# Kernel optimization log

Measured on AMD Instinct MI355X. Metric: run time of the kernel, lower is better.

The kernel has to match this reference:

```python
import jax, jax.numpy as jnp
import numpy as np

B, T, D = 8, 2048, 768
NUM_HEADS, KEY_DIM, VAL_DIM = 12, 64, 64
QKV_OUT = NUM_HEADS * (2 * KEY_DIM + VAL_DIM)  # 2304
MHK = NUM_HEADS * KEY_DIM  # 768


def setup_inputs() -> dict:
    key = jax.random.key(0)
    k = jax.random.split(key, 5)
    x = jax.random.normal(k[0], (B, T, D), dtype=jnp.float32)
    # Linear weights stored as [in, out] (equivalent to torch W.T)
    w_qkv = jax.random.normal(k[1], (D, QKV_OUT), dtype=jnp.float32) * (1.0 / np.sqrt(D))
    b_qkv = jax.random.normal(k[2], (QKV_OUT,), dtype=jnp.float32) * 0.02
    w_out = jax.random.normal(k[3], (NUM_HEADS * VAL_DIM, D), dtype=jnp.float32) * (1.0 / np.sqrt(NUM_HEADS * VAL_DIM))
    b_out = jax.random.normal(k[4], (D,), dtype=jnp.float32) * 0.02
    return {"x": x, "w_qkv": w_qkv, "b_qkv": b_qkv, "w_out": w_out, "b_out": b_out}


def reference(x, w_qkv, b_qkv, w_out, b_out):
    # qkv: [B, T, 2304]
    qkv = jnp.einsum('btd,de->bte', x, w_qkv) + b_qkv
    q = qkv[:, :, :MHK]            # [B, T, 768]
    k = qkv[:, :, MHK:2 * MHK]     # [B, T, 768]
    v = qkv[:, :, 2 * MHK:]        # [B, T, 768]
    # NOTE: faithful to source — contracts over the FULL num_heads*key_dim dim
    # (no head split), scale = sqrt(key_dim) only.
    scores = jnp.einsum('bqd,bkd->bqk', q, k) / jnp.sqrt(jnp.float32(KEY_DIM))
    attn = jax.nn.softmax(scores, axis=-1)        # [B, T, T]
    out = jnp.einsum('bqk,bkd->bqd', attn, v)      # [B, T, 768]
    return jnp.einsum('btd,de->bte', out, w_out) + b_out
```

## Files before the change

kernel.cpp:

```cpp
#include <hip/hip_runtime.h>

#define BB 8
#define TT 2048
#define DD 768
#define EE 2304
#define MM (BB * TT)
#define MHK_ 768
#define LOG2E 1.44269504088896340736f

typedef __attribute__((ext_vector_type(8))) _Float16 f16x8;
typedef __attribute__((ext_vector_type(4))) float f32x4;

typedef const __attribute__((address_space(1))) void* gp_t;
typedef __attribute__((address_space(3))) void* lp_t;

__device__ __forceinline__ float fast_exp2(float x) { return __builtin_amdgcn_exp2f(x); }

__global__ __launch_bounds__(256)
void k_cast(const float* __restrict__ in, _Float16* __restrict__ out, int n8) {
  int idx = blockIdx.x * 256 + threadIdx.x;
  if (idx >= n8) return;
  const float4* p = (const float4*)(in + idx * 8);
  float4 a = p[0], b = p[1];
  f16x8 o;
  o[0] = (_Float16)a.x; o[1] = (_Float16)a.y; o[2] = (_Float16)a.z; o[3] = (_Float16)a.w;
  o[4] = (_Float16)b.x; o[5] = (_Float16)b.y; o[6] = (_Float16)b.z; o[7] = (_Float16)b.w;
  *(f16x8*)(out + idx * 8) = o;
}

__global__ __launch_bounds__(256)
void k_tcast(const float* __restrict__ in, _Float16* __restrict__ out, int R, int C) {
  int idx = blockIdx.x * 256 + threadIdx.x;
  if (idx >= R * C) return;
  int r = idx / C, c = idx - r * C;
  out[(size_t)c * R + r] = (_Float16)in[idx];
}

__global__ __launch_bounds__(256)
void k_vt(const _Float16* __restrict__ qkv, _Float16* __restrict__ Vt) {
  __shared__ _Float16 tile[32][33];
  const int tx = threadIdx.x & 31;
  const int ty = threadIdx.x >> 5;
  const int t0 = blockIdx.x * 32;
  const int d0 = blockIdx.y * 32;
  const int b = blockIdx.z;
  for (int r = 0; r < 4; r++) {
    int t = t0 + ty + r * 8;
    tile[ty + r * 8][tx] = qkv[(size_t)(b * TT + t) * EE + 2 * MHK_ + d0 + tx];
  }
  __syncthreads();
  for (int r = 0; r < 4; r++) {
    int d = d0 + ty + r * 8;
    Vt[((size_t)b * DD + d) * TT + t0 + tx] = tile[tx][ty + r * 8];
  }
}

__global__ __launch_bounds__(256)
void k_softmax(const _Float16* __restrict__ S, _Float16* __restrict__ P) {
  const int row = blockIdx.x;
  const _Float16* s = S + (size_t)row * TT;
  _Float16* p = P + (size_t)row * TT;
  const int tid = threadIdx.x;
  const int lane = tid & 63;
  const int w = tid >> 6;
  __shared__ float redm[4], reds[4];
  f16x8 v = *(const f16x8*)(s + tid * 8);
  float f[8];
  for (int i = 0; i < 8; i++) f[i] = (float)v[i];
  float mx = f[0];
  for (int i = 1; i < 8; i++) mx = fmaxf(mx, f[i]);
  for (int off = 1; off < 64; off <<= 1) mx = fmaxf(mx, __shfl_xor(mx, off, 64));
  if (lane == 0) redm[w] = mx;
  __syncthreads();
  mx = fmaxf(fmaxf(redm[0], redm[1]), fmaxf(redm[2], redm[3]));
  float e[8], ls = 0.f;
  for (int i = 0; i < 8; i++) { e[i] = fast_exp2(f[i] - mx); ls += e[i]; }
  for (int off = 1; off < 64; off <<= 1) ls += __shfl_xor(ls, off, 64);
  if (lane == 0) reds[w] = ls;
  __syncthreads();
  float inv = 1.f / (reds[0] + reds[1] + reds[2] + reds[3]);
  f16x8 o;
  for (int i = 0; i < 8; i++) o[i] = (_Float16)(e[i] * inv);
  *(f16x8*)(p + tid * 8) = o;
}

template<bool OUT_F16, bool HAS_BIAS, bool QSCALE>
__global__ __launch_bounds__(256)
void k_gemm(const _Float16* __restrict__ A, const _Float16* __restrict__ Bt,
            const float* __restrict__ bias, void* __restrict__ Cv,
            int lda, int ldb, int ldc, int Kd,
            long long strideA, long long strideB, long long strideC,
            float qscale) {
  __shared__ __align__(16) _Float16 As[128 * 32];
  __shared__ __align__(16) _Float16 Bs[128 * 32];
  const int tid = threadIdx.x;
  const int lane = tid & 63;
  const int w = tid >> 6;
  const int quad = lane >> 4;
  const int l16 = lane & 15;
  const int m0 = blockIdx.y * 128;
  const int n0 = blockIdx.x * 128;
  const int wr = (w >> 1) * 64;
  const int wc = (w & 1) * 64;

  const int arow = w * 16 + (lane >> 2);
  const int acol = (lane & 3) * 8;

  const _Float16* Ap = A + (long long)blockIdx.z * strideA + (size_t)(m0 + arow) * lda + acol;
  const _Float16* Bp = Bt + (long long)blockIdx.z * strideB + (size_t)(n0 + arow) * ldb + acol;
  const size_t a64 = (size_t)64 * lda;
  const size_t b64 = (size_t)64 * ldb;
  _Float16* ldsA0 = &As[(w * 16) * 32];
  _Float16* ldsA1 = &As[(w * 16 + 64) * 32];
  _Float16* ldsB0 = &Bs[(w * 16) * 32];
  _Float16* ldsB1 = &Bs[(w * 16 + 64) * 32];

  f32x4 acc[4][4];
  for (int i = 0; i < 4; i++)
    for (int j = 0; j < 4; j++)
      for (int r = 0; r < 4; r++) acc[i][j][r] = 0.f;

  for (int kk = 0; kk < Kd; kk += 32) {
    __syncthreads();
    __builtin_amdgcn_global_load_lds((gp_t)(Ap), (lp_t)ldsA0, 16, 0, 0);
    __builtin_amdgcn_global_load_lds((gp_t)(Ap + a64), (lp_t)ldsA1, 16, 0, 0);
    __builtin_amdgcn_global_load_lds((gp_t)(Bp), (lp_t)ldsB0, 16, 0, 0);
    __builtin_amdgcn_global_load_lds((gp_t)(Bp + b64), (lp_t)ldsB1, 16, 0, 0);
    Ap += 32;
    Bp += 32;
    __syncthreads();
    f16x8 af[4], bf[4];
    for (int i = 0; i < 4; i++) af[i] = *(const f16x8*)&As[(wr + i * 16 + l16) * 32 + quad * 8];
    for (int j = 0; j < 4; j++) bf[j] = *(const f16x8*)&Bs[(wc + j * 16 + l16) * 32 + quad * 8];
    for (int i = 0; i < 4; i++)
      for (int j = 0; j < 4; j++)
        acc[i][j] = __builtin_amdgcn_mfma_f32_16x16x32_f16(af[i], bf[j], acc[i][j], 0, 0, 0);
  }

  const long long cbase = (long long)blockIdx.z * strideC;
  for (int j = 0; j < 4; j++) {
    int col = n0 + wc + j * 16 + l16;
    float bv = HAS_BIAS ? bias[col] : 0.f;
    float sc = 1.f;
    if (QSCALE && col < MHK_) sc = qscale;
    for (int i = 0; i < 4; i++) {
      int row = m0 + wr + i * 16 + quad * 4;
      for (int r = 0; r < 4; r++) {
        float v = (acc[i][j][r] + bv) * sc;
        if (OUT_F16)
          ((_Float16*)Cv)[cbase + (size_t)(row + r) * ldc + col] = (_Float16)v;
        else
          ((float*)Cv)[cbase + (size_t)(row + r) * ldc + col] = v;
      }
    }
  }
}

extern "C" void kernel_launch(void* const* d_in, const int* in_sizes, int n_in,
                              void* d_out, int out_size, void* d_ws, size_t ws_size,
                              hipStream_t stream) {
  const float* x = (const float*)d_in[0];
  const float* w_qkv = (const float*)d_in[1];
  const float* b_qkv = (const float*)d_in[2];
  const float* w_out = (const float*)d_in[3];
  const float* b_out = (const float*)d_in[4];

  _Float16* ws = (_Float16*)d_ws;
  _Float16* w_qkvT = ws;
  _Float16* w_outT = w_qkvT + (size_t)EE * DD;
  _Float16* qkv = w_outT + (size_t)DD * DD;
  _Float16* Vt = qkv + (size_t)MM * EE;
  _Float16* S = Vt + (size_t)BB * DD * TT;
  _Float16* P = S + (size_t)BB * TT * TT;
  _Float16* ctx = P + (size_t)BB * TT * TT;
  _Float16* xh = P;

  k_cast<<<(MM * DD / 8 + 255) / 256, 256, 0, stream>>>(x, xh, MM * DD / 8);
  k_tcast<<<(DD * EE + 255) / 256, 256, 0, stream>>>(w_qkv, w_qkvT, DD, EE);
  k_tcast<<<(DD * DD + 255) / 256, 256, 0, stream>>>(w_out, w_outT, DD, DD);
  k_gemm<true, true, true><<<dim3(EE / 128, MM / 128, 1), 256, 0, stream>>>(
      xh, w_qkvT, b_qkv, qkv, DD, DD, EE, DD, 0, 0, 0, 0.125f * LOG2E);
  k_vt<<<dim3(TT / 32, DD / 32, BB), 256, 0, stream>>>(qkv, Vt);
  k_gemm<true, false, false><<<dim3(TT / 128, TT / 128, BB), 256, 0, stream>>>(
      qkv, qkv + MHK_, nullptr, S, EE, EE, TT, DD,
      (long long)TT * EE, (long long)TT * EE, (long long)TT * TT, 1.f);
  k_softmax<<<MM, 256, 0, stream>>>(S, P);
  k_gemm<true, false, false><<<dim3(DD / 128, TT / 128, BB), 256, 0, stream>>>(
      P, Vt, nullptr, ctx, TT, TT, DD, TT,
      (long long)TT * TT, (long long)DD * TT, (long long)TT * DD, 1.f);
  k_gemm<false, true, false><<<dim3(DD / 128, MM / 128, 1), 256, 0, stream>>>(
      ctx, w_outT, b_out, d_out, DD, DD, DD, DD, 0, 0, 0, 1.f);
}
```

Baseline: 447.8 us.

## Merge prep kernels and deepen GEMM K-tile to 64 with XOR-swizzled LDS

```diff
diff --git a/kernel.cpp b/kernel.cpp
--- a/kernel.cpp
+++ b/kernel.cpp
@@ -17,23 +17,27 @@
 __device__ __forceinline__ float fast_exp2(float x) { return __builtin_amdgcn_exp2f(x); }
 
 __global__ __launch_bounds__(256)
-void k_cast(const float* __restrict__ in, _Float16* __restrict__ out, int n8) {
-  int idx = blockIdx.x * 256 + threadIdx.x;
-  if (idx >= n8) return;
-  const float4* p = (const float4*)(in + idx * 8);
-  float4 a = p[0], b = p[1];
-  f16x8 o;
-  o[0] = (_Float16)a.x; o[1] = (_Float16)a.y; o[2] = (_Float16)a.z; o[3] = (_Float16)a.w;
-  o[4] = (_Float16)b.x; o[5] = (_Float16)b.y; o[6] = (_Float16)b.z; o[7] = (_Float16)b.w;
-  *(f16x8*)(out + idx * 8) = o;
-}
-
-__global__ __launch_bounds__(256)
-void k_tcast(const float* __restrict__ in, _Float16* __restrict__ out, int R, int C) {
-  int idx = blockIdx.x * 256 + threadIdx.x;
-  if (idx >= R * C) return;
-  int r = idx / C, c = idx - r * C;
-  out[(size_t)c * R + r] = (_Float16)in[idx];
+void k_prep(const float* __restrict__ x, const float* __restrict__ w_qkv,
+            const float* __restrict__ w_out, _Float16* __restrict__ xh,
+            _Float16* __restrict__ w_qkvT, _Float16* __restrict__ w_outT) {
+  int bid = blockIdx.x;
+  if (bid < 6144) {
+    int idx = bid * 256 + threadIdx.x;
+    const float4* p = (const float4*)(x + idx * 8);
+    float4 a = p[0], b = p[1];
+    f16x8 o;
+    o[0] = (_Float16)a.x; o[1] = (_Float16)a.y; o[2] = (_Float16)a.z; o[3] = (_Float16)a.w;
+    o[4] = (_Float16)b.x; o[5] = (_Float16)b.y; o[6] = (_Float16)b.z; o[7] = (_Float16)b.w;
+    *(f16x8*)(xh + idx * 8) = o;
+  } else if (bid < 6144 + 6912) {
+    int idx = (bid - 6144) * 256 + threadIdx.x;
+    int r = idx / EE, c = idx - r * EE;
+    w_qkvT[(size_t)c * DD + r] = (_Float16)w_qkv[idx];
+  } else {
+    int idx = (bid - 13056) * 256 + threadIdx.x;
+    int r = idx / DD, c = idx - r * DD;
+    w_outT[(size_t)c * DD + r] = (_Float16)w_out[idx];
+  }
 }
 
 __global__ __launch_bounds__(256)
@@ -91,8 +95,8 @@
             int lda, int ldb, int ldc, int Kd,
             long long strideA, long long strideB, long long strideC,
             float qscale) {
-  __shared__ __align__(16) _Float16 As[128 * 32];
-  __shared__ __align__(16) _Float16 Bs[128 * 32];
+  __shared__ __align__(16) _Float16 As[128 * 64];
+  __shared__ __align__(16) _Float16 Bs[128 * 64];
   const int tid = threadIdx.x;
   const int lane = tid & 63;
   const int w = tid >> 6;
@@ -103,38 +107,40 @@
   const int wr = (w >> 1) * 64;
   const int wc = (w & 1) * 64;
 
-  const int arow = w * 16 + (lane >> 2);
-  const int acol = (lane & 3) * 8;
-
-  const _Float16* Ap = A + (long long)blockIdx.z * strideA + (size_t)(m0 + arow) * lda + acol;
-  const _Float16* Bp = Bt + (long long)blockIdx.z * strideB + (size_t)(n0 + arow) * ldb + acol;
-  const size_t a64 = (size_t)64 * lda;
-  const size_t b64 = (size_t)64 * ldb;
-  _Float16* ldsA0 = &As[(w * 16) * 32];
-  _Float16* ldsA1 = &As[(w * 16 + 64) * 32];
-  _Float16* ldsB0 = &Bs[(w * 16) * 32];
-  _Float16* ldsB1 = &Bs[(w * 16 + 64) * 32];
+  const int srow = w * 32 + (lane >> 3);
+  const int scc = ((lane & 7) ^ ((lane >> 3) & 7)) * 8;
+  const _Float16* Ap = A + (long long)blockIdx.z * strideA + (size_t)(m0 + srow) * lda + scc;
+  const _Float16* Bp = Bt + (long long)blockIdx.z * strideB + (size_t)(n0 + srow) * ldb + scc;
+  _Float16* ldsA = &As[(w * 32) * 64];
+  _Float16* ldsB = &Bs[(w * 32) * 64];
 
   f32x4 acc[4][4];
   for (int i = 0; i < 4; i++)
     for (int j = 0; j < 4; j++)
       for (int r = 0; r < 4; r++) acc[i][j][r] = 0.f;
 
-  for (int kk = 0; kk < Kd; kk += 32) {
+  const int swz = (quad ^ (l16 & 7)) * 8;
+
+  for (int kk = 0; kk < Kd; kk += 64) {
     __syncthreads();
-    __builtin_amdgcn_global_load_lds((gp_t)(Ap), (lp_t)ldsA0, 16, 0, 0);
-    __builtin_amdgcn_global_load_lds((gp_t)(Ap + a64), (lp_t)ldsA1, 16, 0, 0);
-    __builtin_amdgcn_global_load_lds((gp_t)(Bp), (lp_t)ldsB0, 16, 0, 0);
-    __builtin_amdgcn_global_load_lds((gp_t)(Bp + b64), (lp_t)ldsB1, 16, 0, 0);
-    Ap += 32;
-    Bp += 32;
+    for (int i = 0; i < 4; i++) {
+      __builtin_amdgcn_global_load_lds((gp_t)(Ap + (size_t)(i * 8) * lda),
+                                       (lp_t)(ldsA + i * 8 * 64), 16, 0, 0);
+      __builtin_amdgcn_global_load_lds((gp_t)(Bp + (size_t)(i * 8) * ldb),
+                                       (lp_t)(ldsB + i * 8 * 64), 16, 0, 0);
+    }
+    Ap += 64;
+    Bp += 64;
     __syncthreads();
-    f16x8 af[4], bf[4];
-    for (int i = 0; i < 4; i++) af[i] = *(const f16x8*)&As[(wr + i * 16 + l16) * 32 + quad * 8];
-    for (int j = 0; j < 4; j++) bf[j] = *(const f16x8*)&Bs[(wc + j * 16 + l16) * 32 + quad * 8];
-    for (int i = 0; i < 4; i++)
-      for (int j = 0; j < 4; j++)
-        acc[i][j] = __builtin_amdgcn_mfma_f32_16x16x32_f16(af[i], bf[j], acc[i][j], 0, 0, 0);
+    for (int s = 0; s < 2; s++) {
+      const int so = swz ^ (s * 32);
+      f16x8 af[4], bf[4];
+      for (int i = 0; i < 4; i++) af[i] = *(const f16x8*)&As[(wr + i * 16 + l16) * 64 + so];
+      for (int j = 0; j < 4; j++) bf[j] = *(const f16x8*)&Bs[(wc + j * 16 + l16) * 64 + so];
+      for (int i = 0; i < 4; i++)
+        for (int j = 0; j < 4; j++)
+          acc[i][j] = __builtin_amdgcn_mfma_f32_16x16x32_f16(af[i], bf[j], acc[i][j], 0, 0, 0);
+    }
   }
 
   const long long cbase = (long long)blockIdx.z * strideC;
@@ -175,9 +181,7 @@
   _Float16* ctx = P + (size_t)BB * TT * TT;
   _Float16* xh = P;
 
-  k_cast<<<(MM * DD / 8 + 255) / 256, 256, 0, stream>>>(x, xh, MM * DD / 8);
-  k_tcast<<<(DD * EE + 255) / 256, 256, 0, stream>>>(w_qkv, w_qkvT, DD, EE);
-  k_tcast<<<(DD * DD + 255) / 256, 256, 0, stream>>>(w_out, w_outT, DD, DD);
+  k_prep<<<15360, 256, 0, stream>>>(x, w_qkv, w_out, xh, w_qkvT, w_outT);
   k_gemm<true, true, true><<<dim3(EE / 128, MM / 128, 1), 256, 0, stream>>>(
       xh, w_qkvT, b_qkv, qkv, DD, DD, EE, DD, 0, 0, 0, 0.125f * LOG2E);
   k_vt<<<dim3(TT / 32, DD / 32, BB), 256, 0, stream>>>(qkv, Vt);
```

After: 430.6 us. 3.8% less time.
